# Performance work log

Measured on AMD Instinct MI355X. Metric: run time of the kernel, lower is better.

Reference implementation:

```python
import jax, jax.numpy as jnp
import numpy as np

B, T, H, W, C = 4, 16, 56, 56, 256
NH = 8
CS = (2, 7, 7)   # cuboid_size
SS = (1, 3, 3)   # shift_size


def _reorder(x):
    # (B,T,H,W,C) -> (B, num_cuboids, cuboid_volume, C), strategy 'lll'
    b = x.shape[0]
    bt, bh, bw = CS
    x = x.reshape(b, T // bt, bt, H // bh, bh, W // bw, bw, C)
    x = x.transpose(0, 1, 3, 5, 2, 4, 6, 7)
    return x.reshape(b, (T // bt) * (H // bh) * (W // bw), bt * bh * bw, C)


def _reorder_rev(x):
    b = x.shape[0]
    bt, bh, bw = CS
    x = x.reshape(b, T // bt, H // bh, W // bw, bt, bh, bw, C)
    x = x.transpose(0, 1, 4, 2, 5, 3, 6, 7)
    return x.reshape(b, T, H, W, C)


def _attn_mask():
    # shift-window mask, computed statically with numpy (no padding needed:
    # T,H,W divide CS exactly, so data_mask is all-ones)
    m = np.zeros((T, H, W))
    cnt = 0
    for t in (slice(-CS[0]), slice(-CS[0], -SS[0]), slice(-SS[0], None)):
        for h in (slice(-CS[1]), slice(-CS[1], -SS[1]), slice(-SS[1], None)):
            for w in (slice(-CS[2]), slice(-CS[2], -SS[2]), slice(-SS[2], None)):
                m[t, h, w] = cnt
                cnt += 1
    bt, bh, bw = CS
    m = m.reshape(T // bt, bt, H // bh, bh, W // bw, bw)
    m = m.transpose(0, 2, 4, 1, 3, 5).reshape(-1, bt * bh * bw)
    return jnp.asarray(m[:, None, :] == m[:, :, None])  # (num_cuboids, vol, vol)


def setup_inputs() -> dict:
    key = jax.random.key(0)
    k1, k2, k3 = jax.random.split(key, 3)
    return {
        "x": jax.random.normal(k1, (B, T, H, W, C), dtype=jnp.float32),
        "gamma": jnp.ones((C,), jnp.float32),
        "beta": jnp.zeros((C,), jnp.float32),
        "w_qkv": jax.random.normal(k2, (3 * C, C), jnp.float32) * 0.02,
        "w_proj": jax.random.normal(k3, (C, C), jnp.float32) * 0.02,
        "b_proj": jnp.zeros((C,), jnp.float32),
    }


def reference(x, gamma, beta, w_qkv, w_proj, b_proj):
    hd = C // NH
    scale = hd ** -0.5
    # pre-norm (LayerNorm, eps=1e-5, biased variance as in torch)
    mu = x.mean(-1, keepdims=True)
    var = x.var(-1, keepdims=True)
    xn = (x - mu) * jax.lax.rsqrt(var + 1e-5) * gamma + beta
    # shift then cuboid reorder
    xs = jnp.roll(xn, shift=(-SS[0], -SS[1], -SS[2]), axis=(1, 2, 3))
    r = _reorder(xs)                       # (B, nc, vol, C)
    nc, vol = r.shape[1], r.shape[2]
    qkv = jnp.einsum('bnvc,dc->bnvd', r, w_qkv).reshape(B, nc, vol, 3, NH, hd)
    qkv = qkv.transpose(3, 0, 4, 1, 2, 5)  # (3, B, NH, nc, vol, hd)
    q, k, v = qkv[0], qkv[1], qkv[2]
    mask = _attn_mask()                    # (nc, vol, vol) bool
    score = jnp.einsum('bhnic,bhnjc->bhnij', q * scale, k)
    score = jnp.where(mask, score, jnp.float32(-1e18))
    attn = jax.nn.softmax(score, axis=-1) * mask  # masked_softmax
    out = jnp.einsum('bhnij,bhnjc->bhnic', attn, v)
    out = out.transpose(0, 2, 3, 1, 4).reshape(B, nc, vol, C)
    out = jnp.einsum('bnvc,dc->bnvd', out, w_proj) + b_proj  # final proj
    y = _reorder_rev(out)
    y = jnp.roll(y, shift=(SS[0], SS[1], SS[2]), axis=(1, 2, 3))
    return y
```

## Files before the change

### kernel.cpp

```cpp
#include <hip/hip_runtime.h>
#include <hip/hip_bf16.h>

#define NC_  512
#define VOL_ 98

typedef __attribute__((ext_vector_type(8))) short bf16x8;
typedef __attribute__((ext_vector_type(4))) float f32x4;
typedef __attribute__((ext_vector_type(16))) float f32x16;
typedef unsigned int u32;
typedef unsigned short u16;

#define MFMA16(a,b,c) __builtin_amdgcn_mfma_f32_16x16x32_bf16((a),(b),(c),0,0,0)
#define MFMA32(a,b,c) __builtin_amdgcn_mfma_f32_32x32x16_bf16((a),(b),(c),0,0,0)

#define SWZ(r)  ((unsigned)((((r) & 7)) << 4))
#define SWZV(d) ((unsigned)(((((d) & 7)) ^ (((d) & 8) >> 1)) << 4))

__device__ __forceinline__ u16 f2bf(float f) {
    u32 u = __float_as_uint(f);
    u32 r = (u + 0x7fffu + ((u >> 16) & 1u)) >> 16;
    return (u16)r;
}
__device__ __forceinline__ u32 cvt_pk(float lo, float hi) {
    u32 r;
    asm("v_cvt_pk_bf16_f32 %0, %1, %2" : "=v"(r) : "v"(lo), "v"(hi));
    return r;
}

__global__ void k_conv(const float* __restrict__ wqkv, const float* __restrict__ wproj,
                       u16* __restrict__ o)
{
    int i = blockIdx.x * 256 + threadIdx.x;
    if (i < 196608) {
        float v = wqkv[i];
        if (i < 65536) v *= 0.17677669529663687f;
        o[i] = f2bf(v);
    } else if (i < 262144) {
        o[i] = f2bf(wproj[i - 196608]);
    }
}

__global__ __launch_bounds__(512, 4)
void k_attn(const float* __restrict__ x, const float* __restrict__ gamma,
            const float* __restrict__ beta, const u16* __restrict__ wbf,
            u16* __restrict__ ao)
{
    __shared__ __align__(16) u16 rn[VOL_ * 256];
    __shared__ __align__(16) u16 Qs[112 * 32];
    __shared__ __align__(16) u16 Ks[112 * 32];
    __shared__ __align__(16) u16 Vt[32 * 128];
    __shared__ u32 rowbase[112];
    __shared__ unsigned char labs[128];

    const int bid = blockIdx.x;
    const int b  = bid >> 9, n = bid & 511;
    const int ti = n >> 6, hi = (n >> 3) & 7, wi = n & 7;
    const int tid = threadIdx.x;
    const int lane = tid & 63, wv = tid >> 6;
    const int c15 = lane & 15, g  = lane >> 4;
    const int c31 = lane & 31, g2 = lane >> 5;

    if (tid < 128) {
        int i = tid;
        int vt = (i >= 49) ? 1 : 0;
        int r  = i - vt * 49;
        int vh = r / 7, vw = r - vh * 7;
        int t = ti * 2 + vt, h = hi * 7 + vh, w = wi * 7 + vw;
        if (i < 112) {
            int ts = (t + 1) & 15;
            int hs = h + 3; if (hs >= 56) hs -= 56;
            int ws2 = w + 3; if (ws2 >= 56) ws2 -= 56;
            rowbase[i] = (i < VOL_) ? (u32)((((b * 16 + ts) * 56 + hs) * 56 + ws2) * 256) : 0u;
        }
        if (i < VOL_) {
            int tr = (t < 14) ? 0 : ((t < 15) ? 1 : 2);
            int hr = (h < 49) ? 0 : ((h < 53) ? 1 : 2);
            int wr = (w < 49) ? 0 : ((w < 53) ? 1 : 2);
            labs[i] = (unsigned char)(tr * 9 + hr * 3 + wr);
        } else {
            labs[i] = (unsigned char)255;
        }
    }
    {
        int d = tid >> 4, k = 112 + (tid & 15);
        unsigned a = (unsigned)(d * 256 + k * 2) ^ SWZV(d);
        *(u16*)((char*)Vt + a) = 0;
    }
    __syncthreads();

    const float4 gm = *(const float4*)(gamma + lane * 4);
    const float4 be = *(const float4*)(beta  + lane * 4);
    for (int i = wv; i < VOL_; i += 8) {
        const float* xp = x + (size_t)rowbase[i] + lane * 4;
        float4 xv = *(const float4*)xp;
        float s  = xv.x + xv.y + xv.z + xv.w;
        float s2 = xv.x * xv.x + xv.y * xv.y + xv.z * xv.z + xv.w * xv.w;
        #pragma unroll
        for (int o = 1; o < 64; o <<= 1) { s += __shfl_xor(s, o); s2 += __shfl_xor(s2, o); }
        float mu  = s  * (1.0f / 256.0f);
        float var = s2 * (1.0f / 256.0f) - mu * mu;
        float rs  = rsqrtf(var + 1e-5f);
        unsigned a = ((unsigned)(i * 512 + lane * 8)) ^ SWZ(i);
        uint2 pk2;
        pk2.x = cvt_pk((xv.x - mu) * rs * gm.x + be.x, (xv.y - mu) * rs * gm.y + be.y);
        pk2.y = cvt_pk((xv.z - mu) * rs * gm.z + be.z, (xv.w - mu) * rs * gm.w + be.w);
        *(uint2*)((char*)rn + a) = pk2;
    }

    u32 lab4[7];
    #pragma unroll
    for (int c = 0; c < 7; ++c) lab4[c] = *(const u32*)&labs[c * 16 + g * 4];

    for (int hh = 0; hh < 8; ++hh) {
        __syncthreads();

        for (int u = wv; u < 12; u += 8) {
            int proj = u >> 2, mt = u & 3;
            int arow = mt * 32 + c31; if (arow > 111) arow = 111;
            const u16* wb = wbf + (size_t)(proj * 256 + hh * 32 + c31) * 256 + g2 * 8;
            f32x16 acc = {0,0,0,0,0,0,0,0,0,0,0,0,0,0,0,0};
            #pragma unroll
            for (int half = 0; half < 2; ++half) {
                bf16x8 Bf[8];
                #pragma unroll
                for (int kk = 0; kk < 8; ++kk)
                    Bf[kk] = *(const bf16x8*)(wb + (half * 8 + kk) * 16);
                #pragma unroll
                for (int kk = 0; kk < 8; ++kk) {
                    unsigned a = (unsigned)(arow * 512 + (half * 8 + kk) * 32 + g2 * 16) ^ SWZ(arow);
                    bf16x8 A = *(const bf16x8*)((const char*)rn + a);
                    acc = MFMA32(A, Bf[kk], acc);
                }
            }
            #pragma unroll
            for (int r = 0; r < 16; ++r) {
                int row  = (r & 3) + 8 * (r >> 2) + 4 * g2;
                int grow = mt * 32 + row;
                if (grow < 112) {
                    if (proj == 2) {
                        float v = (grow < VOL_) ? acc[r] : 0.f;
                        unsigned a = (unsigned)(c31 * 256 + grow * 2) ^ SWZV(c31);
                        *(u16*)((char*)Vt + a) = f2bf(v);
                    } else {
                        char* dst = (char*)((proj == 0) ? Qs : Ks);
                        unsigned a = (unsigned)(grow * 64 + c31 * 2) ^ SWZ(grow);
                        *(u16*)(dst + a) = f2bf(acc[r]);
                    }
                }
            }
        }
        __syncthreads();

        for (int mt = wv; mt < 7; mt += 8) {
            int qrow = mt * 16 + c15;
            int labr = labs[qrow];
            u32 labr4 = (u32)labr * 0x01010101u;
            unsigned qa = (unsigned)(qrow * 64 + g * 16) ^ SWZ(qrow);
            bf16x8 qB = *(const bf16x8*)((const char*)Qs + qa);

            f32x4 s[7];
            #pragma unroll
            for (int c = 0; c < 7; ++c) {
                int krow = c * 16 + c15;
                unsigned ka = (unsigned)(krow * 64 + g * 16) ^ SWZ(krow);
                bf16x8 kA = *(const bf16x8*)((const char*)Ks + ka);
                f32x4 z = {0.f, 0.f, 0.f, 0.f};
                s[c] = MFMA16(kA, qB, z);
            }
            float mx = -1e30f;
            #pragma unroll
            for (int c = 0; c < 7; ++c) {
                u32 xo = lab4[c] ^ labr4;
                #pragma unroll
                for (int i = 0; i < 4; ++i) {
                    bool ok = ((xo >> (8 * i)) & 255u) == 0u;
                    mx = fmaxf(mx, ok ? s[c][i] : -1e30f);
                }
            }
            mx = fmaxf(mx, __shfl_xor(mx, 16));
            mx = fmaxf(mx, __shfl_xor(mx, 32));
            float lsum = 0.f;
            #pragma unroll
            for (int c = 0; c < 7; ++c) {
                u32 xo = lab4[c] ^ labr4;
                #pragma unroll
                for (int i = 0; i < 4; ++i) {
                    bool ok = ((xo >> (8 * i)) & 255u) == 0u;
                    float e = ok ? __expf(s[c][i] - mx) : 0.f;
                    s[c][i] = e;
                    lsum += e;
                }
            }
            lsum += __shfl_xor(lsum, 16);
            lsum += __shfl_xor(lsum, 32);
            float inv = 1.0f / lsum;
            u32 pk[8][2];
            #pragma unroll
            for (int c = 0; c < 7; ++c) {
                pk[c][0] = cvt_pk(s[c][0] * inv, s[c][1] * inv);
                pk[c][1] = cvt_pk(s[c][2] * inv, s[c][3] * inv);
            }
            pk[7][0] = 0u; pk[7][1] = 0u;

            f32x4 O0 = {0.f, 0.f, 0.f, 0.f}, O1 = {0.f, 0.f, 0.f, 0.f};
            const int src0 = c15 + 32 * (g & 1);
            const bool csel = (g >> 1) != 0;
            #pragma unroll
            for (int f = 0; f < 4; ++f) {
                union { bf16x8 v; u32 w[4]; } pa;
                #pragma unroll
                for (int w = 0; w < 4; ++w) {
                    int src = src0 + 16 * (w >> 1);
                    u32 r0 = (u32)__shfl((int)pk[2 * f][w & 1], src);
                    u32 r1 = (u32)__shfl((int)pk[2 * f + 1][w & 1], src);
                    pa.w[w] = csel ? r1 : r0;
                }
                unsigned av0 = (unsigned)(c15 * 256 + f * 64 + g * 16) ^ SWZV(c15);
                unsigned av1 = (unsigned)((16 + c15) * 256 + f * 64 + g * 16) ^ SWZV(16 + c15);
                bf16x8 vB0 = *(const bf16x8*)((const char*)Vt + av0);
                bf16x8 vB1 = *(const bf16x8*)((const char*)Vt + av1);
                O0 = MFMA16(pa.v, vB0, O0);
                O1 = MFMA16(pa.v, vB1, O1);
            }
            #pragma unroll
            for (int i = 0; i < 4; ++i) {
                int grow = mt * 16 + g * 4 + i;
                if (grow < VOL_) {
                    size_t base = ((size_t)bid * VOL_ + grow) * 256 + hh * 32;
                    ao[base + c15]      = f2bf(O0[i]);
                    ao[base + 16 + c15] = f2bf(O1[i]);
                }
            }
        }
    }
}

__global__ __launch_bounds__(512, 4)
void k_proj(const u16* __restrict__ ao, const u16* __restrict__ wpbf,
            const float* __restrict__ bp, float* __restrict__ y)
{
    __shared__ __align__(16) u16 tile[VOL_ * 256];
    __shared__ u32 rowbase[112];
    const int bid = blockIdx.x;
    const int b  = bid >> 9, n = bid & 511;
    const int ti = n >> 6, hi = (n >> 3) & 7, wi = n & 7;
    const int tid = threadIdx.x;
    const int c31 = (tid & 63) & 31, g2 = (tid & 63) >> 5;
    const int wv = tid >> 6;

    if (tid < 112) {
        int i = tid;
        int vt = (i >= 49) ? 1 : 0;
        int r  = i - vt * 49;
        int vh = r / 7, vw = r - vh * 7;
        int t = ti * 2 + vt, h = hi * 7 + vh, w = wi * 7 + vw;
        int ts = (t + 1) & 15;
        int hs = h + 3; if (hs >= 56) hs -= 56;
        int ws2 = w + 3; if (ws2 >= 56) ws2 -= 56;
        rowbase[i] = (i < VOL_) ? (u32)((((b * 16 + ts) * 56 + hs) * 56 + ws2) * 256) : 0u;
    }
    const uint4* src = (const uint4*)(ao + (size_t)bid * (VOL_ * 256));
    for (int cidx = tid; cidx < (VOL_ * 256) / 8; cidx += 512) {
        uint4 v = src[cidx];
        int row = cidx >> 5, blk = cidx & 31;
        unsigned a = (unsigned)((row << 9) + (blk << 4)) ^ SWZ(row);
        *(uint4*)((char*)tile + a) = v;
    }
    __syncthreads();

    for (int u = wv; u < 32; u += 8) {
        int nt = u >> 2, mt = u & 3;
        int arow = mt * 32 + c31; if (arow > 97) arow = 97;
        const u16* wb = wpbf + (size_t)(nt * 32 + c31) * 256 + g2 * 8;
        f32x16 acc = {0,0,0,0,0,0,0,0,0,0,0,0,0,0,0,0};
        #pragma unroll
        for (int half = 0; half < 2; ++half) {
            bf16x8 Bf[8];
            #pragma unroll
            for (int kk = 0; kk < 8; ++kk)
                Bf[kk] = *(const bf16x8*)(wb + (half * 8 + kk) * 16);
            #pragma unroll
            for (int kk = 0; kk < 8; ++kk) {
                unsigned a = (unsigned)(arow * 512 + (half * 8 + kk) * 32 + g2 * 16) ^ SWZ(arow);
                bf16x8 A = *(const bf16x8*)((const char*)tile + a);
                acc = MFMA32(A, Bf[kk], acc);
            }
        }
        float bias = bp[nt * 32 + c31];
        #pragma unroll
        for (int r = 0; r < 16; ++r) {
            int row = (r & 3) + 8 * (r >> 2) + 4 * g2 + mt * 32;
            if (row < VOL_) {
                y[(size_t)rowbase[row] + nt * 32 + c31] = acc[r] + bias;
            }
        }
    }
}

extern "C" void kernel_launch(void* const* d_in, const int* in_sizes, int n_in,
                              void* d_out, int out_size, void* d_ws, size_t ws_size,
                              hipStream_t stream) {
    const float* x     = (const float*)d_in[0];
    const float* gamma = (const float*)d_in[1];
    const float* beta  = (const float*)d_in[2];
    const float* wqkv  = (const float*)d_in[3];
    const float* wproj = (const float*)d_in[4];
    const float* bproj = (const float*)d_in[5];
    float* y = (float*)d_out;

    u16* wbf  = (u16*)d_ws;
    u16* wpbf = wbf + 196608;
    u16* ao   = wbf + 262144;

    k_conv<<<dim3(1024), dim3(256), 0, stream>>>(wqkv, wproj, wbf);
    k_attn<<<dim3(4 * NC_), dim3(512), 0, stream>>>(x, gamma, beta, wbf, ao);
    k_proj<<<dim3(4 * NC_), dim3(512), 0, stream>>>(ao, wpbf, bproj, y);
}
```

Before: 625.2 us.

## Fuse output projection into attention kernel and remap block order

Merges the separate projection kernel into the end of the attention kernel. After each block writes its attention output to global memory, it fences, synchronizes, and reads those rows back from global (likely L2-resident) to run the projection MFMA directly, with no LDS staging tile. This removes one kernel launch and the extra pass over the intermediate. It also permutes the block index so consecutive hardware blocks are spread across cuboids, which may change cache and XCD locality. The projection A-operand reads now come from global memory rather than swizzled LDS, which may cost latency.

```diff
diff --git a/kernel.cpp b/kernel.cpp
--- a/kernel.cpp
+++ b/kernel.cpp
@@ -13,7 +13,7 @@
 #define MFMA16(a,b,c) __builtin_amdgcn_mfma_f32_16x16x32_bf16((a),(b),(c),0,0,0)
 #define MFMA32(a,b,c) __builtin_amdgcn_mfma_f32_32x32x16_bf16((a),(b),(c),0,0,0)
 
-#define SWZ(r)  ((unsigned)((((r) & 7)) << 4))
+#define SWZ(r)  ((unsigned)(((r) & 7) << 4))
 #define SWZV(d) ((unsigned)(((((d) & 7)) ^ (((d) & 8) >> 1)) << 4))
 
 __device__ __forceinline__ u16 f2bf(float f) {
@@ -43,7 +43,8 @@
 __global__ __launch_bounds__(512, 4)
 void k_attn(const float* __restrict__ x, const float* __restrict__ gamma,
             const float* __restrict__ beta, const u16* __restrict__ wbf,
-            u16* __restrict__ ao)
+            u16* __restrict__ ao, const u16* __restrict__ wpbf,
+            const float* __restrict__ bp, float* __restrict__ y)
 {
     __shared__ __align__(16) u16 rn[VOL_ * 256];
     __shared__ __align__(16) u16 Qs[112 * 32];
@@ -52,7 +53,8 @@
     __shared__ u32 rowbase[112];
     __shared__ unsigned char labs[128];
 
-    const int bid = blockIdx.x;
+    const int rawb = blockIdx.x;
+    const int bid = ((rawb & 7) << 8) | (rawb >> 3);
     const int b  = bid >> 9, n = bid & 511;
     const int ti = n >> 6, hi = (n >> 3) & 7, wi = n & 7;
     const int tid = threadIdx.x;
@@ -233,44 +235,13 @@
             }
         }
     }
-}
-
-__global__ __launch_bounds__(512, 4)
-void k_proj(const u16* __restrict__ ao, const u16* __restrict__ wpbf,
-            const float* __restrict__ bp, float* __restrict__ y)
-{
-    __shared__ __align__(16) u16 tile[VOL_ * 256];
-    __shared__ u32 rowbase[112];
-    const int bid = blockIdx.x;
-    const int b  = bid >> 9, n = bid & 511;
-    const int ti = n >> 6, hi = (n >> 3) & 7, wi = n & 7;
-    const int tid = threadIdx.x;
-    const int c31 = (tid & 63) & 31, g2 = (tid & 63) >> 5;
-    const int wv = tid >> 6;
-
-    if (tid < 112) {
-        int i = tid;
-        int vt = (i >= 49) ? 1 : 0;
-        int r  = i - vt * 49;
-        int vh = r / 7, vw = r - vh * 7;
-        int t = ti * 2 + vt, h = hi * 7 + vh, w = wi * 7 + vw;
-        int ts = (t + 1) & 15;
-        int hs = h + 3; if (hs >= 56) hs -= 56;
-        int ws2 = w + 3; if (ws2 >= 56) ws2 -= 56;
-        rowbase[i] = (i < VOL_) ? (u32)((((b * 16 + ts) * 56 + hs) * 56 + ws2) * 256) : 0u;
-    }
-    const uint4* src = (const uint4*)(ao + (size_t)bid * (VOL_ * 256));
-    for (int cidx = tid; cidx < (VOL_ * 256) / 8; cidx += 512) {
-        uint4 v = src[cidx];
-        int row = cidx >> 5, blk = cidx & 31;
-        unsigned a = (unsigned)((row << 9) + (blk << 4)) ^ SWZ(row);
-        *(uint4*)((char*)tile + a) = v;
-    }
+
+    __threadfence();
     __syncthreads();
-
     for (int u = wv; u < 32; u += 8) {
         int nt = u >> 2, mt = u & 3;
         int arow = mt * 32 + c31; if (arow > 97) arow = 97;
+        const u16* ap = ao + ((size_t)bid * VOL_ + arow) * 256 + g2 * 8;
         const u16* wb = wpbf + (size_t)(nt * 32 + c31) * 256 + g2 * 8;
         f32x16 acc = {0,0,0,0,0,0,0,0,0,0,0,0,0,0,0,0};
         #pragma unroll
@@ -281,8 +252,7 @@
                 Bf[kk] = *(const bf16x8*)(wb + (half * 8 + kk) * 16);
             #pragma unroll
             for (int kk = 0; kk < 8; ++kk) {
-                unsigned a = (unsigned)(arow * 512 + (half * 8 + kk) * 32 + g2 * 16) ^ SWZ(arow);
-                bf16x8 A = *(const bf16x8*)((const char*)tile + a);
+                bf16x8 A = *(const bf16x8*)(ap + (half * 8 + kk) * 16);
                 acc = MFMA32(A, Bf[kk], acc);
             }
         }
@@ -313,6 +283,5 @@
     u16* ao   = wbf + 262144;
 
     k_conv<<<dim3(1024), dim3(256), 0, stream>>>(wqkv, wproj, wbf);
-    k_attn<<<dim3(4 * NC_), dim3(512), 0, stream>>>(x, gamma, beta, wbf, ao);
-    k_proj<<<dim3(4 * NC_), dim3(512), 0, stream>>>(ao, wpbf, bproj, y);
-}
+    k_attn<<<dim3(4 * NC_), dim3(512), 0, stream>>>(x, gamma, beta, wbf, ao, wpbf, bproj, y);
+}
```

Measured after the change: 1.103 ms. 76.4% more time.

## Widen LDS swizzles, pack V-transpose stores, and remap block order for XCDs

Applied to the files above, without the earlier changes.

The row swizzle on the normalized-input and projection tiles is widened from 3 to 5 bits, and the V-transpose swizzle becomes a plain 4-bit XOR, both to cut LDS bank conflicts on the MFMA operand reads. V writes are packed as pairs of bf16 into 32-bit stores, halving the number of LDS store instructions. Block indices are permuted so consecutive hardware block IDs spread across the 8 XCDs, which is meant to improve L2 locality. The swizzle changes must stay consistent between the writers and readers of each buffer, including the unseen attention section that reads Vt.

```diff
diff --git a/kernel.cpp b/kernel.cpp
--- a/kernel.cpp
+++ b/kernel.cpp
@@ -13,8 +13,9 @@
 #define MFMA16(a,b,c) __builtin_amdgcn_mfma_f32_16x16x32_bf16((a),(b),(c),0,0,0)
 #define MFMA32(a,b,c) __builtin_amdgcn_mfma_f32_32x32x16_bf16((a),(b),(c),0,0,0)
 
-#define SWZ(r)  ((unsigned)((((r) & 7)) << 4))
-#define SWZV(d) ((unsigned)(((((d) & 7)) ^ (((d) & 8) >> 1)) << 4))
+#define SWZ(r)   ((unsigned)(((r) & 7) << 4))
+#define SWZ5(r)  ((unsigned)(((r) & 31) << 4))
+#define SWZV(d)  ((unsigned)(((d) & 15) << 4))
 
 __device__ __forceinline__ u16 f2bf(float f) {
     u32 u = __float_as_uint(f);
@@ -52,7 +53,8 @@
     __shared__ u32 rowbase[112];
     __shared__ unsigned char labs[128];
 
-    const int bid = blockIdx.x;
+    const int rawb = blockIdx.x;
+    const int bid = ((rawb & 7) << 8) | (rawb >> 3);
     const int b  = bid >> 9, n = bid & 511;
     const int ti = n >> 6, hi = (n >> 3) & 7, wi = n & 7;
     const int tid = threadIdx.x;
@@ -81,10 +83,10 @@
             labs[i] = (unsigned char)255;
         }
     }
-    {
-        int d = tid >> 4, k = 112 + (tid & 15);
-        unsigned a = (unsigned)(d * 256 + k * 2) ^ SWZV(d);
-        *(u16*)((char*)Vt + a) = 0;
+    if (tid < 256) {
+        int d = tid >> 3, kp = 112 + (tid & 7) * 2;
+        unsigned a = (unsigned)(d * 256 + kp * 2) ^ SWZV(d);
+        *(u32*)((char*)Vt + a) = 0u;
     }
     __syncthreads();
 
@@ -100,7 +102,7 @@
         float mu  = s  * (1.0f / 256.0f);
         float var = s2 * (1.0f / 256.0f) - mu * mu;
         float rs  = rsqrtf(var + 1e-5f);
-        unsigned a = ((unsigned)(i * 512 + lane * 8)) ^ SWZ(i);
+        unsigned a = ((unsigned)(i * 512 + lane * 8)) ^ SWZ5(i);
         uint2 pk2;
         pk2.x = cvt_pk((xv.x - mu) * rs * gm.x + be.x, (xv.y - mu) * rs * gm.y + be.y);
         pk2.y = cvt_pk((xv.z - mu) * rs * gm.z + be.z, (xv.w - mu) * rs * gm.w + be.w);
@@ -127,22 +129,26 @@
                     Bf[kk] = *(const bf16x8*)(wb + (half * 8 + kk) * 16);
                 #pragma unroll
                 for (int kk = 0; kk < 8; ++kk) {
-                    unsigned a = (unsigned)(arow * 512 + (half * 8 + kk) * 32 + g2 * 16) ^ SWZ(arow);
+                    unsigned a = (unsigned)(arow * 512 + (half * 8 + kk) * 32 + g2 * 16) ^ SWZ5(arow);
                     bf16x8 A = *(const bf16x8*)((const char*)rn + a);
                     acc = MFMA32(A, Bf[kk], acc);
                 }
             }
-            #pragma unroll
-            for (int r = 0; r < 16; ++r) {
-                int row  = (r & 3) + 8 * (r >> 2) + 4 * g2;
-                int grow = mt * 32 + row;
-                if (grow < 112) {
-                    if (proj == 2) {
-                        float v = (grow < VOL_) ? acc[r] : 0.f;
-                        unsigned a = (unsigned)(c31 * 256 + grow * 2) ^ SWZV(c31);
-                        *(u16*)((char*)Vt + a) = f2bf(v);
-                    } else {
-                        char* dst = (char*)((proj == 0) ? Qs : Ks);
+            if (proj == 2) {
+                #pragma unroll
+                for (int r = 0; r < 16; r += 2) {
+                    int kpos = mt * 32 + (r & 3) + 8 * (r >> 2) + 4 * g2;
+                    float v0 = (kpos < VOL_)     ? acc[r]     : 0.f;
+                    float v1 = (kpos + 1 < VOL_) ? acc[r + 1] : 0.f;
+                    unsigned a = (unsigned)(c31 * 256 + kpos * 2) ^ SWZV(c31);
+                    *(u32*)((char*)Vt + a) = cvt_pk(v0, v1);
+                }
+            } else {
+                char* dst = (char*)((proj == 0) ? Qs : Ks);
+                #pragma unroll
+                for (int r = 0; r < 16; ++r) {
+                    int grow = mt * 32 + (r & 3) + 8 * (r >> 2) + 4 * g2;
+                    if (grow < 112) {
                         unsigned a = (unsigned)(grow * 64 + c31 * 2) ^ SWZ(grow);
                         *(u16*)(dst + a) = f2bf(acc[r]);
                     }
@@ -241,7 +247,8 @@
 {
     __shared__ __align__(16) u16 tile[VOL_ * 256];
     __shared__ u32 rowbase[112];
-    const int bid = blockIdx.x;
+    const int rawb = blockIdx.x;
+    const int bid = ((rawb & 7) << 8) | (rawb >> 3);
     const int b  = bid >> 9, n = bid & 511;
     const int ti = n >> 6, hi = (n >> 3) & 7, wi = n & 7;
     const int tid = threadIdx.x;
@@ -263,7 +270,7 @@
     for (int cidx = tid; cidx < (VOL_ * 256) / 8; cidx += 512) {
         uint4 v = src[cidx];
         int row = cidx >> 5, blk = cidx & 31;
-        unsigned a = (unsigned)((row << 9) + (blk << 4)) ^ SWZ(row);
+        unsigned a = (unsigned)((row << 9) + (blk << 4)) ^ SWZ5(row);
         *(uint4*)((char*)tile + a) = v;
     }
     __syncthreads();
@@ -281,7 +288,7 @@
                 Bf[kk] = *(const bf16x8*)(wb + (half * 8 + kk) * 16);
             #pragma unroll
             for (int kk = 0; kk < 8; ++kk) {
-                unsigned a = (unsigned)(arow * 512 + (half * 8 + kk) * 32 + g2 * 16) ^ SWZ(arow);
+                unsigned a = (unsigned)(arow * 512 + (half * 8 + kk) * 32 + g2 * 16) ^ SWZ5(arow);
                 bf16x8 A = *(const bf16x8*)((const char*)tile + a);
                 acc = MFMA32(A, Bf[kk], acc);
             }
```

Measured after the change: 613.1 us. About the same (-1.9%).
